# Kernel tuning notes

Hardware: AMD Instinct MI355X
Metric: run time of the kernel (lower is better)

Reference implementation:

```python
import jax, jax.numpy as jnp
import numpy as np

NUM_HEADS = 16
D_K = 64
D_V = 64
D_MODEL = 1024


def setup_inputs() -> dict:
    key = jax.random.key(0)
    ks = jax.random.split(key, 11)
    B, S = 2, 2048
    s = 0.02
    return {
        "Q": jax.random.normal(ks[0], (B, S, D_MODEL), jnp.float32),
        "K": jax.random.normal(ks[1], (B, S, D_MODEL), jnp.float32),
        "V": jax.random.normal(ks[2], (B, S, D_MODEL), jnp.float32),
        "WQ": jax.random.normal(ks[3], (D_MODEL, NUM_HEADS * D_K), jnp.float32) * s,
        "bQ": jnp.zeros((NUM_HEADS * D_K,), jnp.float32),
        "WK": jax.random.normal(ks[4], (D_MODEL, NUM_HEADS * D_K), jnp.float32) * s,
        "bK": jnp.zeros((NUM_HEADS * D_K,), jnp.float32),
        "WV": jax.random.normal(ks[5], (D_MODEL, NUM_HEADS * D_V), jnp.float32) * s,
        "bV": jnp.zeros((NUM_HEADS * D_V,), jnp.float32),
        "WO": jax.random.normal(ks[6], (NUM_HEADS * D_V, D_MODEL), jnp.float32) * s,
        "bO": jnp.zeros((D_MODEL,), jnp.float32),
    }


def reference(Q, K, V, WQ, bQ, WK, bK, WV, bV, WO, bO):
    B = Q.shape[0]
    # linear projections, then split heads: [B, H, S, d]
    q = (Q @ WQ + bQ).reshape(B, -1, NUM_HEADS, D_K).transpose(0, 2, 1, 3)
    k = (K @ WK + bK).reshape(B, -1, NUM_HEADS, D_K).transpose(0, 2, 1, 3)
    v = (V @ WV + bV).reshape(B, -1, NUM_HEADS, D_V).transpose(0, 2, 1, 3)
    # unfused attention: full [B, H, Sq, Sk] score matrix
    scores = jnp.einsum("bhqd,bhkd->bhqk", q, k) / jnp.sqrt(jnp.float32(D_K))
    attn = jax.nn.softmax(scores, axis=-1)  # dropout is identity in eval mode
    out = jnp.einsum("bhqk,bhkd->bhqd", attn, v)
    out = out.transpose(0, 2, 1, 3).reshape(B, -1, NUM_HEADS * D_V)
    return out @ WO + bO
```

## Files before the change

### kernel.cpp

```cpp
#include <hip/hip_runtime.h>
#include <hip/hip_bf16.h>
#include <stdint.h>

#define BATCH 2
#define SEQ   2048
#define NH    16
#define DH    64
#define DM    1024
#define MR    (BATCH * SEQ)

typedef __bf16 bf16_t;
typedef bf16_t bf16x4 __attribute__((ext_vector_type(4)));
typedef bf16_t bf16x8 __attribute__((ext_vector_type(8)));
typedef float  f32x4  __attribute__((ext_vector_type(4)));
typedef float  f32x16 __attribute__((ext_vector_type(16)));

typedef const __attribute__((address_space(1))) void* gas_t;
typedef       __attribute__((address_space(3))) void* las_t;

__device__ __forceinline__ void gload16(const void* g, void* l) {
  __builtin_amdgcn_global_load_lds((gas_t)g, (las_t)l, 16, 0, 0);
}

__device__ __forceinline__ float fast_exp2(float x) {
#if __has_builtin(__builtin_amdgcn_exp2f)
  return __builtin_amdgcn_exp2f(x);
#else
  float r; asm volatile("v_exp_f32 %0, %1\n\ts_nop 1" : "=v"(r) : "v"(x)); return r;
#endif
}

__global__ __launch_bounds__(256) void cvt3_kernel(const float* __restrict__ x0,
                                                   const float* __restrict__ x1,
                                                   const float* __restrict__ x2,
                                                   bf16_t* __restrict__ y0,
                                                   bf16_t* __restrict__ y1,
                                                   bf16_t* __restrict__ y2, int n) {
  const int z = blockIdx.y;
  const float* x = z == 0 ? x0 : (z == 1 ? x1 : x2);
  bf16_t*      y = z == 0 ? y0 : (z == 1 ? y1 : y2);
  int i = (blockIdx.x * 256 + threadIdx.x) * 8;
  if (i + 8 <= n) {
    float4 a = *(const float4*)(x + i);
    float4 b = *(const float4*)(x + i + 4);
    bf16x8 o;
    o[0] = (bf16_t)a.x; o[1] = (bf16_t)a.y; o[2] = (bf16_t)a.z; o[3] = (bf16_t)a.w;
    o[4] = (bf16_t)b.x; o[5] = (bf16_t)b.y; o[6] = (bf16_t)b.z; o[7] = (bf16_t)b.w;
    *(bf16x8*)(y + i) = o;
  }
}

__global__ __launch_bounds__(256) void wtrans4_kernel(const float* __restrict__ W0,
                                                      const float* __restrict__ W1,
                                                      const float* __restrict__ W2,
                                                      const float* __restrict__ W3,
                                                      bf16_t* __restrict__ T0,
                                                      bf16_t* __restrict__ T1,
                                                      bf16_t* __restrict__ T2,
                                                      bf16_t* __restrict__ T3) {
  const int z = blockIdx.z;
  const float* W = z == 0 ? W0 : (z == 1 ? W1 : (z == 2 ? W2 : W3));
  bf16_t*     Wt = z == 0 ? T0 : (z == 1 ? T1 : (z == 2 ? T2 : T3));
  __shared__ bf16_t t[64][65];
  const int c0 = blockIdx.x * 64, r0 = blockIdx.y * 64;
  const int tid = threadIdx.x;
  const int r = tid >> 2, cc = (tid & 3) * 16;
  const float* src = W + (size_t)(r0 + r) * DM + c0 + cc;
#pragma unroll
  for (int i = 0; i < 16; ++i) t[r][cc + i] = (bf16_t)src[i];
  __syncthreads();
  bf16_t* dst = Wt + (size_t)(c0 + r) * DM + r0 + cc;
#pragma unroll
  for (int i = 0; i < 16; ++i) dst[i] = t[cc + i][r];
}

__global__ __launch_bounds__(256) void gemm3_kernel(
    const bf16_t* __restrict__ A0, const bf16_t* __restrict__ A1,
    const bf16_t* __restrict__ A2,
    const bf16_t* __restrict__ B0, const bf16_t* __restrict__ B1,
    const bf16_t* __restrict__ B2,
    const float* __restrict__ bi0, const float* __restrict__ bi1,
    const float* __restrict__ bi2,
    float s0, float s1, float s2,
    bf16_t* __restrict__ C0, bf16_t* __restrict__ C1, bf16_t* __restrict__ C2) {
  const int z = blockIdx.z;
  const bf16_t* A    = z == 0 ? A0 : (z == 1 ? A1 : A2);
  const bf16_t* Bt   = z == 0 ? B0 : (z == 1 ? B1 : B2);
  const float*  bias = z == 0 ? bi0 : (z == 1 ? bi1 : bi2);
  const float   scale = z == 0 ? s0 : (z == 1 ? s1 : s2);
  bf16_t*       C    = z == 0 ? C0 : (z == 1 ? C1 : C2);
  const int K = DM, N = DM;

  __shared__ __attribute__((aligned(16))) bf16_t As[128 * 64];
  __shared__ __attribute__((aligned(16))) bf16_t Bs[128 * 64];
  const int m0 = blockIdx.x * 128, n0 = blockIdx.y * 128;
  const int tid = threadIdx.x;
  const int wave = tid >> 6, lane = tid & 63;
  const int lm = lane & 15, lg = lane >> 4;
  const int wr = wave >> 1, wc = wave & 1;
  f32x4 acc[4][4];
#pragma unroll
  for (int a = 0; a < 4; ++a)
#pragma unroll
    for (int bb = 0; bb < 4; ++bb) acc[a][bb] = (f32x4){0.f, 0.f, 0.f, 0.f};

  for (int k0 = 0; k0 < K; k0 += 64) {
    __syncthreads();
#pragma unroll
    for (int i = 0; i < 4; ++i) {
      const int c = tid + i * 256;
      const int row = c >> 3, j = c & 7, js = j ^ (row & 7);
      gload16(A  + (size_t)(m0 + row) * K + k0 + js * 8,
              As + (size_t)(wave * 64 + i * 256) * 8);
      gload16(Bt + (size_t)(n0 + row) * K + k0 + js * 8,
              Bs + (size_t)(wave * 64 + i * 256) * 8);
    }
    asm volatile("s_waitcnt vmcnt(0)" ::: "memory");
    __syncthreads();
#pragma unroll
    for (int kk = 0; kk < 2; ++kk) {
      bf16x8 af[4], bfr[4];
#pragma unroll
      for (int t = 0; t < 4; ++t) {
        const int ra = wr * 64 + t * 16 + lm;
        af[t] = *(const bf16x8*)((const char*)As + ra * 128 +
                                 ((kk * 64 + lg * 16) ^ ((ra & 7) << 4)));
        const int rb = wc * 64 + t * 16 + lm;
        bfr[t] = *(const bf16x8*)((const char*)Bs + rb * 128 +
                                  ((kk * 64 + lg * 16) ^ ((rb & 7) << 4)));
      }
      __builtin_amdgcn_s_setprio(1);
#pragma unroll
      for (int mf = 0; mf < 4; ++mf)
#pragma unroll
        for (int nf = 0; nf < 4; ++nf)
          acc[mf][nf] = __builtin_amdgcn_mfma_f32_16x16x32_bf16(af[mf], bfr[nf],
                                                                acc[mf][nf], 0, 0, 0);
      __builtin_amdgcn_s_setprio(0);
    }
  }
#pragma unroll
  for (int mf = 0; mf < 4; ++mf)
#pragma unroll
    for (int nf = 0; nf < 4; ++nf) {
      const int col = n0 + wc * 64 + nf * 16 + lm;
      const float bv = bias[col];
#pragma unroll
      for (int i = 0; i < 4; ++i) {
        const int row = m0 + wr * 64 + mf * 16 + lg * 4 + i;
        const float val = (acc[mf][nf][i] + bv) * scale;
        size_t off;
        if (z == 0) {
          off = (size_t)row * N + col;
        } else {
          const int bb = row >> 11, s = row & (SEQ - 1);
          const int hh = col >> 6, d = col & 63;
          const size_t base = (size_t)(bb * NH + hh) * (SEQ * DH);
          if (z == 1) {
            off = base + ((((size_t)(s >> 6) * 2 + ((s >> 5) & 1)) * 4 + (d >> 4)) * 64
                          + ((d >> 3) & 1) * 32 + (s & 31)) * 8 + (d & 7);
          } else {
            off = base + ((((size_t)(s >> 6) * 2 + (d >> 5)) * 4 + ((s >> 4) & 3)) * 64
                          + ((s >> 3) & 1) * 32 + (d & 31)) * 8 + (s & 7);
          }
        }
        C[off] = (bf16_t)val;
      }
    }
}

template <int OUT_BF16>
__global__ __launch_bounds__(256) void gemm_kernel(const bf16_t* __restrict__ A,
                                                   const bf16_t* __restrict__ Bt,
                                                   const float* __restrict__ bias,
                                                   float scale,
                                                   void* __restrict__ Cv,
                                                   int K, int N) {
  __shared__ __attribute__((aligned(16))) bf16_t As[64 * 64];
  __shared__ __attribute__((aligned(16))) bf16_t Bs[128 * 64];
  const int m0 = blockIdx.x * 64, n0 = blockIdx.y * 128;
  const int tid = threadIdx.x;
  const int wave = tid >> 6, lane = tid & 63;
  const int lm = lane & 15, lg = lane >> 4;
  const int wr = wave >> 1, wc = wave & 1;
  f32x4 acc[2][4];
#pragma unroll
  for (int a = 0; a < 2; ++a)
#pragma unroll
    for (int bb = 0; bb < 4; ++bb) acc[a][bb] = (f32x4){0.f, 0.f, 0.f, 0.f};

  for (int k0 = 0; k0 < K; k0 += 64) {
    __syncthreads();
#pragma unroll
    for (int i = 0; i < 2; ++i) {
      const int c = tid + i * 256;
      const int row = c >> 3, j = c & 7, js = j ^ (row & 7);
      gload16(A + (size_t)(m0 + row) * K + k0 + js * 8,
              As + (size_t)(wave * 64 + i * 256) * 8);
    }
#pragma unroll
    for (int i = 0; i < 4; ++i) {
      const int c = tid + i * 256;
      const int row = c >> 3, j = c & 7, js = j ^ (row & 7);
      gload16(Bt + (size_t)(n0 + row) * K + k0 + js * 8,
              Bs + (size_t)(wave * 64 + i * 256) * 8);
    }
    asm volatile("s_waitcnt vmcnt(0)" ::: "memory");
    __syncthreads();
#pragma unroll
    for (int kk = 0; kk < 2; ++kk) {
      bf16x8 af[2], bfr[4];
#pragma unroll
      for (int t = 0; t < 2; ++t) {
        const int ra = wr * 32 + t * 16 + lm;
        af[t] = *(const bf16x8*)((const char*)As + ra * 128 +
                                 ((kk * 64 + lg * 16) ^ ((ra & 7) << 4)));
      }
#pragma unroll
      for (int t = 0; t < 4; ++t) {
        const int rb = wc * 64 + t * 16 + lm;
        bfr[t] = *(const bf16x8*)((const char*)Bs + rb * 128 +
                                  ((kk * 64 + lg * 16) ^ ((rb & 7) << 4)));
      }
      __builtin_amdgcn_s_setprio(1);
#pragma unroll
      for (int mf = 0; mf < 2; ++mf)
#pragma unroll
        for (int nf = 0; nf < 4; ++nf)
          acc[mf][nf] = __builtin_amdgcn_mfma_f32_16x16x32_bf16(af[mf], bfr[nf],
                                                                acc[mf][nf], 0, 0, 0);
      __builtin_amdgcn_s_setprio(0);
    }
  }
#pragma unroll
  for (int mf = 0; mf < 2; ++mf)
#pragma unroll
    for (int nf = 0; nf < 4; ++nf) {
      const int col = n0 + wc * 64 + nf * 16 + lm;
      const float bv = bias[col];
#pragma unroll
      for (int i = 0; i < 4; ++i) {
        const int row = m0 + wr * 32 + mf * 16 + lg * 4 + i;
        const float val = (acc[mf][nf][i] + bv) * scale;
        if (OUT_BF16) ((bf16_t*)Cv)[(size_t)row * N + col] = (bf16_t)val;
        else          ((float*)Cv)[(size_t)row * N + col] = val;
      }
    }
}

__device__ __forceinline__ void attn_iter5(const bf16x8 (&kf)[8],
                                           const bf16x8 (&qf)[4],
                                           const bf16_t* __restrict__ vbt,
                                           f32x16 (&acc0)[2],
                                           float& mrun, float& lrun,
                                           char* __restrict__ PsW,
                                           int lq, int hi, int lane) {
  bf16x8 vf[8];
#pragma unroll
  for (int i = 0; i < 8; ++i) vf[i] = *(const bf16x8*)(vbt + i * 512);

  f32x16 sc[2];
#pragma unroll
  for (int r = 0; r < 16; ++r) { sc[0][r] = 0.f; sc[1][r] = 0.f; }
  __builtin_amdgcn_s_setprio(1);
#pragma unroll
  for (int ds = 0; ds < 4; ++ds) {
    sc[0] = __builtin_amdgcn_mfma_f32_32x32x16_bf16(kf[ds],     qf[ds], sc[0], 0, 0, 0);
    sc[1] = __builtin_amdgcn_mfma_f32_32x32x16_bf16(kf[4 + ds], qf[ds], sc[1], 0, 0, 0);
  }
  __builtin_amdgcn_s_setprio(0);

  float ml = sc[0][0];
#pragma unroll
  for (int r = 1; r < 16; ++r) ml = fmaxf(ml, sc[0][r]);
#pragma unroll
  for (int r = 0; r < 16; ++r) ml = fmaxf(ml, sc[1][r]);
  ml = fmaxf(ml, __shfl_xor(ml, 32));
  const bool defer = __all(ml - mrun <= 8.0f);
  const float mn = defer ? mrun : fmaxf(mrun, ml);
#pragma unroll
  for (int kt = 0; kt < 2; ++kt)
#pragma unroll
    for (int r = 0; r < 16; ++r) sc[kt][r] = fast_exp2(sc[kt][r] - mn);
  float s = 0.f;
#pragma unroll
  for (int r = 0; r < 16; ++r) s += sc[0][r] + sc[1][r];
  s += __shfl_xor(s, 32);
  if (defer) {
    lrun += s;
  } else {
    const float alpha = fast_exp2(mrun - mn);
    mrun = mn;
    lrun = lrun * alpha + s;
#pragma unroll
    for (int r = 0; r < 16; ++r) {
      const float ar = __shfl(alpha, (r & 3) + 8 * (r >> 2) + 4 * hi);
      acc0[0][r] *= ar;
      acc0[1][r] *= ar;
    }
  }

#pragma unroll
  for (int kt = 0; kt < 2; ++kt)
#pragma unroll
    for (int g = 0; g < 4; ++g) {
      bf16x4 pw;
      pw[0] = (bf16_t)sc[kt][4 * g + 0]; pw[1] = (bf16_t)sc[kt][4 * g + 1];
      pw[2] = (bf16_t)sc[kt][4 * g + 2]; pw[3] = (bf16_t)sc[kt][4 * g + 3];
      *(bf16x4*)(PsW + lq * 128 +
                 ((kt * 64 + g * 16 + hi * 8) ^ ((lq & 7) << 4))) = pw;
    }

#pragma unroll
  for (int ks = 0; ks < 4; ++ks) {
    bf16x8 pf = *(const bf16x8*)(PsW + lq * 128 +
                                 ((ks * 32 + hi * 16) ^ ((lq & 7) << 4)));
    __builtin_amdgcn_s_setprio(1);
    acc0[0] = __builtin_amdgcn_mfma_f32_32x32x16_bf16(pf, vf[ks],     acc0[0], 0, 0, 0);
    acc0[1] = __builtin_amdgcn_mfma_f32_32x32x16_bf16(pf, vf[4 + ks], acc0[1], 0, 0, 0);
    __builtin_amdgcn_s_setprio(0);
  }
}

__global__ __launch_bounds__(256, 2) void flash_kernel(const bf16_t* __restrict__ q,
                                                       const bf16_t* __restrict__ kF,
                                                       const bf16_t* __restrict__ vF,
                                                       bf16_t* __restrict__ o) {
  __shared__ __attribute__((aligned(16))) bf16_t Ps[4][32 * 64];
  const int wg = blockIdx.x;
  const int swz = (wg & 7) * 64 + (wg >> 3);
  const int qt = swz & 15, h = (swz >> 4) & 15, b = swz >> 8;
  const int tid = threadIdx.x;
  const int wave = tid >> 6, lane = tid & 63;
  const int lq = lane & 31, hi = lane >> 5;
  char* PsW = (char*)(&Ps[wave][0]);

  const bf16_t* qb = q + (size_t)(b * SEQ + qt * 128 + wave * 32) * DM + h * DH;
  const bf16_t* kb = kF + (size_t)(b * NH + h) * (SEQ * DH) + lane * 8;
  const bf16_t* vb = vF + (size_t)(b * NH + h) * (SEQ * DH) + lane * 8;

  bf16x8 qf[4];
#pragma unroll
  for (int ds = 0; ds < 4; ++ds)
    qf[ds] = *(const bf16x8*)(qb + (size_t)lq * DM + ds * 16 + hi * 8);

  f32x16 acc[2];
#pragma unroll
  for (int r = 0; r < 16; ++r) { acc[0][r] = 0.f; acc[1][r] = 0.f; }
  float mrun = -1e30f, lrun = 0.f;

  bf16x8 kfA[8], kfB[8];
#pragma unroll
  for (int i = 0; i < 8; ++i) kfA[i] = *(const bf16x8*)(kb + i * 512);

  const int NT = SEQ / 64;
  for (int t = 0; t < NT; t += 2) {
#pragma unroll
    for (int i = 0; i < 8; ++i)
      kfB[i] = *(const bf16x8*)(kb + (size_t)(t + 1) * 4096 + i * 512);
    attn_iter5(kfA, qf, vb + (size_t)t * 4096, acc, mrun, lrun, PsW, lq, hi, lane);
    {
      const int tn = (t + 2 < NT) ? t + 2 : NT - 1;
#pragma unroll
      for (int i = 0; i < 8; ++i)
        kfA[i] = *(const bf16x8*)(kb + (size_t)tn * 4096 + i * 512);
    }
    attn_iter5(kfB, qf, vb + (size_t)(t + 1) * 4096, acc, mrun, lrun, PsW, lq, hi, lane);
  }

  const float inv = __builtin_amdgcn_rcpf(lrun);
#pragma unroll
  for (int r = 0; r < 16; ++r) {
    const int qrow = (r & 3) + 8 * (r >> 2) + 4 * hi;
    const float iv = __shfl(inv, qrow);
    const int row = b * SEQ + qt * 128 + wave * 32 + qrow;
#pragma unroll
    for (int dt = 0; dt < 2; ++dt) {
      const int col = h * DH + dt * 32 + lq;
      o[(size_t)row * DM + col] = (bf16_t)(acc[dt][r] * iv);
    }
  }
}

extern "C" void kernel_launch(void* const* d_in, const int* in_sizes, int n_in,
                              void* d_out, int out_size, void* d_ws, size_t ws_size,
                              hipStream_t stream) {
  (void)in_sizes; (void)n_in; (void)out_size; (void)ws_size;
  const float* Q  = (const float*)d_in[0];
  const float* Kx = (const float*)d_in[1];
  const float* V  = (const float*)d_in[2];
  const float* WQ = (const float*)d_in[3];
  const float* bQ = (const float*)d_in[4];
  const float* WK = (const float*)d_in[5];
  const float* bK = (const float*)d_in[6];
  const float* WV = (const float*)d_in[7];
  const float* bV = (const float*)d_in[8];
  const float* WO = (const float*)d_in[9];
  const float* bO = (const float*)d_in[10];

  const size_t MS  = (size_t)MR * DM;
  const size_t WSZ = (size_t)DM * DM;
  bf16_t* ws  = (bf16_t*)d_ws;
  bf16_t* Qb  = ws;
  bf16_t* Kb  = Qb + MS;
  bf16_t* Vb  = Kb + MS;
  bf16_t* WQt = Vb + MS;
  bf16_t* WKt = WQt + WSZ;
  bf16_t* WVt = WKt + WSZ;
  bf16_t* WOt = WVt + WSZ;
  bf16_t* qp  = WOt + WSZ;
  bf16_t* kp  = qp + MS;
  bf16_t* vp  = kp + MS;
  bf16_t* ao  = Kb;

  const float scale_q = 0.125f * 1.44269504088896340736f;

  cvt3_kernel<<<dim3((unsigned)(MS / 2048), 3), 256, 0, stream>>>(Q, Kx, V, Qb, Kb, Vb, (int)MS);
  wtrans4_kernel<<<dim3(16, 16, 4), 256, 0, stream>>>(WQ, WK, WV, WO, WQt, WKt, WVt, WOt);

  gemm3_kernel<<<dim3(32, 8, 3), 256, 0, stream>>>(Qb, Kb, Vb,
                                                   WQt, WKt, WVt,
                                                   bQ, bK, bV,
                                                   scale_q, 1.0f, 1.0f,
                                                   qp, kp, vp);

  flash_kernel<<<dim3(512), 256, 0, stream>>>(qp, kp, vp, ao);
  gemm_kernel<0><<<dim3(MR / 64, DM / 128), 256, 0, stream>>>(ao, WOt, bO, 1.0f, d_out, DM, DM);
}
```

Measured before the change: 132.7 us.

## Fuse fp32-to-bf16 input conversion into QKV GEMM and pipeline flash K/V loads

```diff
diff --git a/kernel.cpp b/kernel.cpp
--- a/kernel.cpp
+++ b/kernel.cpp
@@ -30,25 +30,10 @@
 #endif
 }
 
-__global__ __launch_bounds__(256) void cvt3_kernel(const float* __restrict__ x0,
-                                                   const float* __restrict__ x1,
-                                                   const float* __restrict__ x2,
-                                                   bf16_t* __restrict__ y0,
-                                                   bf16_t* __restrict__ y1,
-                                                   bf16_t* __restrict__ y2, int n) {
-  const int z = blockIdx.y;
-  const float* x = z == 0 ? x0 : (z == 1 ? x1 : x2);
-  bf16_t*      y = z == 0 ? y0 : (z == 1 ? y1 : y2);
-  int i = (blockIdx.x * 256 + threadIdx.x) * 8;
-  if (i + 8 <= n) {
-    float4 a = *(const float4*)(x + i);
-    float4 b = *(const float4*)(x + i + 4);
-    bf16x8 o;
-    o[0] = (bf16_t)a.x; o[1] = (bf16_t)a.y; o[2] = (bf16_t)a.z; o[3] = (bf16_t)a.w;
-    o[4] = (bf16_t)b.x; o[5] = (bf16_t)b.y; o[6] = (bf16_t)b.z; o[7] = (bf16_t)b.w;
-    *(bf16x8*)(y + i) = o;
-  }
-}
+#define GL(dst, base, OFF) \
+  asm volatile("global_load_dwordx4 %0, %1, off offset:" #OFF : "=v"(dst) : "v"(base))
+#define WAITV(N) asm volatile("s_waitcnt vmcnt(" #N ")" ::: "memory")
+#define SCHED0 __builtin_amdgcn_sched_barrier(0)
 
 __global__ __launch_bounds__(256) void wtrans4_kernel(const float* __restrict__ W0,
                                                       const float* __restrict__ W1,
@@ -75,8 +60,8 @@
 }
 
 __global__ __launch_bounds__(256) void gemm3_kernel(
-    const bf16_t* __restrict__ A0, const bf16_t* __restrict__ A1,
-    const bf16_t* __restrict__ A2,
+    const float* __restrict__ A0, const float* __restrict__ A1,
+    const float* __restrict__ A2,
     const bf16_t* __restrict__ B0, const bf16_t* __restrict__ B1,
     const bf16_t* __restrict__ B2,
     const float* __restrict__ bi0, const float* __restrict__ bi1,
@@ -84,14 +69,14 @@
     float s0, float s1, float s2,
     bf16_t* __restrict__ C0, bf16_t* __restrict__ C1, bf16_t* __restrict__ C2) {
   const int z = blockIdx.z;
-  const bf16_t* A    = z == 0 ? A0 : (z == 1 ? A1 : A2);
+  const float*  A    = z == 0 ? A0 : (z == 1 ? A1 : A2);
   const bf16_t* Bt   = z == 0 ? B0 : (z == 1 ? B1 : B2);
   const float*  bias = z == 0 ? bi0 : (z == 1 ? bi1 : bi2);
   const float   scale = z == 0 ? s0 : (z == 1 ? s1 : s2);
   bf16_t*       C    = z == 0 ? C0 : (z == 1 ? C1 : C2);
   const int K = DM, N = DM;
 
-  __shared__ __attribute__((aligned(16))) bf16_t As[128 * 64];
+  __shared__ __attribute__((aligned(16))) float  As[128 * 64];
   __shared__ __attribute__((aligned(16))) bf16_t Bs[128 * 64];
   const int m0 = blockIdx.x * 128, n0 = blockIdx.y * 128;
   const int tid = threadIdx.x;
@@ -107,11 +92,16 @@
   for (int k0 = 0; k0 < K; k0 += 64) {
     __syncthreads();
 #pragma unroll
+    for (int i = 0; i < 8; ++i) {
+      const int c = tid + i * 256;
+      const int row = c >> 4, j = c & 15, js = j ^ (row & 15);
+      gload16(A + (size_t)(m0 + row) * K + k0 + js * 4,
+              As + (size_t)(wave * 64 + i * 256) * 4);
+    }
+#pragma unroll
     for (int i = 0; i < 4; ++i) {
       const int c = tid + i * 256;
       const int row = c >> 3, j = c & 7, js = j ^ (row & 7);
-      gload16(A  + (size_t)(m0 + row) * K + k0 + js * 8,
-              As + (size_t)(wave * 64 + i * 256) * 8);
       gload16(Bt + (size_t)(n0 + row) * K + k0 + js * 8,
               Bs + (size_t)(wave * 64 + i * 256) * 8);
     }
@@ -123,8 +113,15 @@
 #pragma unroll
       for (int t = 0; t < 4; ++t) {
         const int ra = wr * 64 + t * 16 + lm;
-        af[t] = *(const bf16x8*)((const char*)As + ra * 128 +
-                                 ((kk * 64 + lg * 16) ^ ((ra & 7) << 4)));
+        const char* arow = (const char*)As + ra * 256;
+        const int ca = kk * 8 + lg * 2;
+        f32x4 a0 = *(const f32x4*)(arow + (((ca    ) ^ (ra & 15)) << 4));
+        f32x4 a1 = *(const f32x4*)(arow + (((ca + 1) ^ (ra & 15)) << 4));
+#pragma unroll
+        for (int jj = 0; jj < 4; ++jj) {
+          af[t][jj]     = (bf16_t)a0[jj];
+          af[t][4 + jj] = (bf16_t)a1[jj];
+        }
         const int rb = wc * 64 + t * 16 + lm;
         bfr[t] = *(const bf16x8*)((const char*)Bs + rb * 128 +
                                   ((kk * 64 + lg * 16) ^ ((rb & 7) << 4)));
@@ -248,17 +245,18 @@
     }
 }
 
-__device__ __forceinline__ void attn_iter5(const bf16x8 (&kf)[8],
-                                           const bf16x8 (&qf)[4],
-                                           const bf16_t* __restrict__ vbt,
-                                           f32x16 (&acc0)[2],
-                                           float& mrun, float& lrun,
-                                           char* __restrict__ PsW,
-                                           int lq, int hi, int lane) {
-  bf16x8 vf[8];
-#pragma unroll
-  for (int i = 0; i < 8; ++i) vf[i] = *(const bf16x8*)(vbt + i * 512);
-
+__device__ __forceinline__ void issue8(bf16x8 (&f)[8], const bf16_t* p) {
+  const bf16_t* p2 = p + 2048;
+  GL(f[0], p, 0); GL(f[1], p, 1024); GL(f[2], p, 2048); GL(f[3], p, 3072);
+  GL(f[4], p2, 0); GL(f[5], p2, 1024); GL(f[6], p2, 2048); GL(f[7], p2, 3072);
+}
+
+__device__ __forceinline__ void qk_softmax_store(const bf16x8 (&kf)[8],
+                                                 const bf16x8 (&qf)[4],
+                                                 f32x16 (&acc)[2],
+                                                 float& mrun, float& lrun,
+                                                 char* __restrict__ PsW,
+                                                 int lq, int hi) {
   f32x16 sc[2];
 #pragma unroll
   for (int r = 0; r < 16; ++r) { sc[0][r] = 0.f; sc[1][r] = 0.f; }
@@ -295,8 +293,8 @@
 #pragma unroll
     for (int r = 0; r < 16; ++r) {
       const float ar = __shfl(alpha, (r & 3) + 8 * (r >> 2) + 4 * hi);
-      acc0[0][r] *= ar;
-      acc0[1][r] *= ar;
+      acc[0][r] *= ar;
+      acc[1][r] *= ar;
     }
   }
 
@@ -310,14 +308,17 @@
       *(bf16x4*)(PsW + lq * 128 +
                  ((kt * 64 + g * 16 + hi * 8) ^ ((lq & 7) << 4))) = pw;
     }
-
+}
+
+__device__ __forceinline__ void pv_step(const bf16x8 (&vf)[8], f32x16 (&acc)[2],
+                                        char* __restrict__ PsW, int lq, int hi) {
 #pragma unroll
   for (int ks = 0; ks < 4; ++ks) {
     bf16x8 pf = *(const bf16x8*)(PsW + lq * 128 +
                                  ((ks * 32 + hi * 16) ^ ((lq & 7) << 4)));
     __builtin_amdgcn_s_setprio(1);
-    acc0[0] = __builtin_amdgcn_mfma_f32_32x32x16_bf16(pf, vf[ks],     acc0[0], 0, 0, 0);
-    acc0[1] = __builtin_amdgcn_mfma_f32_32x32x16_bf16(pf, vf[4 + ks], acc0[1], 0, 0, 0);
+    acc[0] = __builtin_amdgcn_mfma_f32_32x32x16_bf16(pf, vf[ks],     acc[0], 0, 0, 0);
+    acc[1] = __builtin_amdgcn_mfma_f32_32x32x16_bf16(pf, vf[4 + ks], acc[1], 0, 0, 0);
     __builtin_amdgcn_s_setprio(0);
   }
 }
@@ -349,24 +350,28 @@
   for (int r = 0; r < 16; ++r) { acc[0][r] = 0.f; acc[1][r] = 0.f; }
   float mrun = -1e30f, lrun = 0.f;
 
-  bf16x8 kfA[8], kfB[8];
-#pragma unroll
-  for (int i = 0; i < 8; ++i) kfA[i] = *(const bf16x8*)(kb + i * 512);
+  bf16x8 kA[8], kB[8], vv[8];
+  issue8(kA, kb);
 
   const int NT = SEQ / 64;
   for (int t = 0; t < NT; t += 2) {
-#pragma unroll
-    for (int i = 0; i < 8; ++i)
-      kfB[i] = *(const bf16x8*)(kb + (size_t)(t + 1) * 4096 + i * 512);
-    attn_iter5(kfA, qf, vb + (size_t)t * 4096, acc, mrun, lrun, PsW, lq, hi, lane);
+    issue8(vv, vb + (size_t)t * 4096);
+    issue8(kB, kb + (size_t)(t + 1) * 4096);
+    WAITV(16); SCHED0;
+    qk_softmax_store(kA, qf, acc, mrun, lrun, PsW, lq, hi);
+    WAITV(8); SCHED0;
+    pv_step(vv, acc, PsW, lq, hi);
+    issue8(vv, vb + (size_t)(t + 1) * 4096);
     {
       const int tn = (t + 2 < NT) ? t + 2 : NT - 1;
-#pragma unroll
-      for (int i = 0; i < 8; ++i)
-        kfA[i] = *(const bf16x8*)(kb + (size_t)tn * 4096 + i * 512);
-    }
-    attn_iter5(kfB, qf, vb + (size_t)(t + 1) * 4096, acc, mrun, lrun, PsW, lq, hi, lane);
-  }
+      issue8(kA, kb + (size_t)tn * 4096);
+    }
+    WAITV(16); SCHED0;
+    qk_softmax_store(kB, qf, acc, mrun, lrun, PsW, lq, hi);
+    WAITV(8); SCHED0;
+    pv_step(vv, acc, PsW, lq, hi);
+  }
+  asm volatile("s_waitcnt vmcnt(0)" ::: "memory");
 
   const float inv = __builtin_amdgcn_rcpf(lrun);
 #pragma unroll
@@ -401,24 +406,20 @@
   const size_t MS  = (size_t)MR * DM;
   const size_t WSZ = (size_t)DM * DM;
   bf16_t* ws  = (bf16_t*)d_ws;
-  bf16_t* Qb  = ws;
-  bf16_t* Kb  = Qb + MS;
-  bf16_t* Vb  = Kb + MS;
-  bf16_t* WQt = Vb + MS;
+  bf16_t* WQt = ws;
   bf16_t* WKt = WQt + WSZ;
   bf16_t* WVt = WKt + WSZ;
   bf16_t* WOt = WVt + WSZ;
   bf16_t* qp  = WOt + WSZ;
   bf16_t* kp  = qp + MS;
   bf16_t* vp  = kp + MS;
-  bf16_t* ao  = Kb;
+  bf16_t* ao  = vp + MS;
 
   const float scale_q = 0.125f * 1.44269504088896340736f;
 
-  cvt3_kernel<<<dim3((unsigned)(MS / 2048), 3), 256, 0, stream>>>(Q, Kx, V, Qb, Kb, Vb, (int)MS);
   wtrans4_kernel<<<dim3(16, 16, 4), 256, 0, stream>>>(WQ, WK, WV, WO, WQt, WKt, WVt, WOt);
 
-  gemm3_kernel<<<dim3(32, 8, 3), 256, 0, stream>>>(Qb, Kb, Vb,
+  gemm3_kernel<<<dim3(32, 8, 3), 256, 0, stream>>>(Q, Kx, V,
                                                    WQt, WKt, WVt,
                                                    bQ, bK, bV,
                                                    scale_q, 1.0f, 1.0f,
```

Result: slower. 138.8 us (+4.6%).

## Split attention over key range with LDS-staged K/V and combine kernel

Applied to the files above, without the earlier changes.

```diff
diff --git a/kernel.cpp b/kernel.cpp
--- a/kernel.cpp
+++ b/kernel.cpp
@@ -8,6 +8,7 @@
 #define DH    64
 #define DM    1024
 #define MR    (BATCH * SEQ)
+#define BHS   65536
 
 typedef __bf16 bf16_t;
 typedef bf16_t bf16x4 __attribute__((ext_vector_type(4)));
@@ -29,6 +30,8 @@
   float r; asm volatile("v_exp_f32 %0, %1\n\ts_nop 1" : "=v"(r) : "v"(x)); return r;
 #endif
 }
+
+#define WAITV(N) asm volatile("s_waitcnt vmcnt(" #N ")" ::: "memory")
 
 __global__ __launch_bounds__(256) void cvt3_kernel(const float* __restrict__ x0,
                                                    const float* __restrict__ x1,
@@ -248,28 +251,10 @@
     }
 }
 
-__device__ __forceinline__ void attn_iter5(const bf16x8 (&kf)[8],
-                                           const bf16x8 (&qf)[4],
-                                           const bf16_t* __restrict__ vbt,
-                                           f32x16 (&acc0)[2],
-                                           float& mrun, float& lrun,
-                                           char* __restrict__ PsW,
-                                           int lq, int hi, int lane) {
-  bf16x8 vf[8];
-#pragma unroll
-  for (int i = 0; i < 8; ++i) vf[i] = *(const bf16x8*)(vbt + i * 512);
-
-  f32x16 sc[2];
-#pragma unroll
-  for (int r = 0; r < 16; ++r) { sc[0][r] = 0.f; sc[1][r] = 0.f; }
-  __builtin_amdgcn_s_setprio(1);
-#pragma unroll
-  for (int ds = 0; ds < 4; ++ds) {
-    sc[0] = __builtin_amdgcn_mfma_f32_32x32x16_bf16(kf[ds],     qf[ds], sc[0], 0, 0, 0);
-    sc[1] = __builtin_amdgcn_mfma_f32_32x32x16_bf16(kf[4 + ds], qf[ds], sc[1], 0, 0, 0);
-  }
-  __builtin_amdgcn_s_setprio(0);
-
+__device__ __forceinline__ void softmax_store(f32x16 (&sc)[2], f32x16 (&acc)[2],
+                                              float& mrun, float& lrun,
+                                              char* __restrict__ PsW,
+                                              int lq, int hi) {
   float ml = sc[0][0];
 #pragma unroll
   for (int r = 1; r < 16; ++r) ml = fmaxf(ml, sc[0][r]);
@@ -295,11 +280,10 @@
 #pragma unroll
     for (int r = 0; r < 16; ++r) {
       const float ar = __shfl(alpha, (r & 3) + 8 * (r >> 2) + 4 * hi);
-      acc0[0][r] *= ar;
-      acc0[1][r] *= ar;
-    }
-  }
-
+      acc[0][r] *= ar;
+      acc[1][r] *= ar;
+    }
+  }
 #pragma unroll
   for (int kt = 0; kt < 2; ++kt)
 #pragma unroll
@@ -310,34 +294,28 @@
       *(bf16x4*)(PsW + lq * 128 +
                  ((kt * 64 + g * 16 + hi * 8) ^ ((lq & 7) << 4))) = pw;
     }
-
-#pragma unroll
-  for (int ks = 0; ks < 4; ++ks) {
-    bf16x8 pf = *(const bf16x8*)(PsW + lq * 128 +
-                                 ((ks * 32 + hi * 16) ^ ((lq & 7) << 4)));
-    __builtin_amdgcn_s_setprio(1);
-    acc0[0] = __builtin_amdgcn_mfma_f32_32x32x16_bf16(pf, vf[ks],     acc0[0], 0, 0, 0);
-    acc0[1] = __builtin_amdgcn_mfma_f32_32x32x16_bf16(pf, vf[4 + ks], acc0[1], 0, 0, 0);
-    __builtin_amdgcn_s_setprio(0);
-  }
-}
-
-__global__ __launch_bounds__(256, 2) void flash_kernel(const bf16_t* __restrict__ q,
+}
+
+__global__ __launch_bounds__(256, 4) void flash_kernel(const bf16_t* __restrict__ q,
                                                        const bf16_t* __restrict__ kF,
                                                        const bf16_t* __restrict__ vF,
-                                                       bf16_t* __restrict__ o) {
-  __shared__ __attribute__((aligned(16))) bf16_t Ps[4][32 * 64];
+                                                       bf16_t* __restrict__ pacc,
+                                                       float* __restrict__ pml) {
+  __shared__ __attribute__((aligned(16))) bf16_t Ks[4096];
+  __shared__ __attribute__((aligned(16))) bf16_t Vs[4096];
+  __shared__ __attribute__((aligned(16))) bf16_t Ps[4][2048];
   const int wg = blockIdx.x;
-  const int swz = (wg & 7) * 64 + (wg >> 3);
-  const int qt = swz & 15, h = (swz >> 4) & 15, b = swz >> 8;
+  const int flat = (wg & 7) * 128 + (wg >> 3);
+  const int qt = flat & 15, h = (flat >> 4) & 15;
+  const int b = (flat >> 8) & 1, split = flat >> 9;
   const int tid = threadIdx.x;
   const int wave = tid >> 6, lane = tid & 63;
   const int lq = lane & 31, hi = lane >> 5;
   char* PsW = (char*)(&Ps[wave][0]);
 
   const bf16_t* qb = q + (size_t)(b * SEQ + qt * 128 + wave * 32) * DM + h * DH;
-  const bf16_t* kb = kF + (size_t)(b * NH + h) * (SEQ * DH) + lane * 8;
-  const bf16_t* vb = vF + (size_t)(b * NH + h) * (SEQ * DH) + lane * 8;
+  const bf16_t* ksrc = kF + (size_t)(b * NH + h) * (SEQ * DH) + tid * 8;
+  const bf16_t* vsrc = vF + (size_t)(b * NH + h) * (SEQ * DH) + tid * 8;
 
   bf16x8 qf[4];
 #pragma unroll
@@ -349,37 +327,83 @@
   for (int r = 0; r < 16; ++r) { acc[0][r] = 0.f; acc[1][r] = 0.f; }
   float mrun = -1e30f, lrun = 0.f;
 
-  bf16x8 kfA[8], kfB[8];
-#pragma unroll
-  for (int i = 0; i < 8; ++i) kfA[i] = *(const bf16x8*)(kb + i * 512);
-
-  const int NT = SEQ / 64;
-  for (int t = 0; t < NT; t += 2) {
-#pragma unroll
-    for (int i = 0; i < 8; ++i)
-      kfB[i] = *(const bf16x8*)(kb + (size_t)(t + 1) * 4096 + i * 512);
-    attn_iter5(kfA, qf, vb + (size_t)t * 4096, acc, mrun, lrun, PsW, lq, hi, lane);
-    {
-      const int tn = (t + 2 < NT) ? t + 2 : NT - 1;
-#pragma unroll
-      for (int i = 0; i < 8; ++i)
-        kfA[i] = *(const bf16x8*)(kb + (size_t)tn * 4096 + i * 512);
-    }
-    attn_iter5(kfB, qf, vb + (size_t)(t + 1) * 4096, acc, mrun, lrun, PsW, lq, hi, lane);
-  }
-
-  const float inv = __builtin_amdgcn_rcpf(lrun);
+  const int t0 = split * 16, tend = t0 + 16;
+
+  for (int t = t0; t < tend; ++t) {
+    gload16(ksrc + (size_t)t * 4096,        &Ks[wave * 512]);
+    gload16(ksrc + (size_t)t * 4096 + 2048, &Ks[2048 + wave * 512]);
+    gload16(vsrc + (size_t)t * 4096,        &Vs[wave * 512]);
+    gload16(vsrc + (size_t)t * 4096 + 2048, &Vs[2048 + wave * 512]);
+    WAITV(0);
+    __builtin_amdgcn_s_barrier();
+    asm volatile("" ::: "memory");
+
+    const char* Kb_ = (const char*)Ks;
+    const char* Vb_ = (const char*)Vs;
+
+    f32x16 sc[2];
+#pragma unroll
+    for (int r = 0; r < 16; ++r) { sc[0][r] = 0.f; sc[1][r] = 0.f; }
+    __builtin_amdgcn_s_setprio(1);
+#pragma unroll
+    for (int ds = 0; ds < 4; ++ds) {
+      bf16x8 k0 = *(const bf16x8*)(Kb_ + (0 * 4 + ds) * 1024 + lane * 16);
+      bf16x8 k1 = *(const bf16x8*)(Kb_ + (1 * 4 + ds) * 1024 + lane * 16);
+      sc[0] = __builtin_amdgcn_mfma_f32_32x32x16_bf16(k0, qf[ds], sc[0], 0, 0, 0);
+      sc[1] = __builtin_amdgcn_mfma_f32_32x32x16_bf16(k1, qf[ds], sc[1], 0, 0, 0);
+    }
+    __builtin_amdgcn_s_setprio(0);
+
+    softmax_store(sc, acc, mrun, lrun, PsW, lq, hi);
+
+#pragma unroll
+    for (int ks = 0; ks < 4; ++ks) {
+      bf16x8 pf = *(const bf16x8*)(PsW + lq * 128 +
+                                   ((ks * 32 + hi * 16) ^ ((lq & 7) << 4)));
+      bf16x8 v0 = *(const bf16x8*)(Vb_ + (0 * 4 + ks) * 1024 + lane * 16);
+      bf16x8 v1 = *(const bf16x8*)(Vb_ + (1 * 4 + ks) * 1024 + lane * 16);
+      __builtin_amdgcn_s_setprio(1);
+      acc[0] = __builtin_amdgcn_mfma_f32_32x32x16_bf16(pf, v0, acc[0], 0, 0, 0);
+      acc[1] = __builtin_amdgcn_mfma_f32_32x32x16_bf16(pf, v1, acc[1], 0, 0, 0);
+      __builtin_amdgcn_s_setprio(0);
+    }
+    asm volatile("" ::: "memory");
+    __builtin_amdgcn_s_barrier();
+  }
+
+  const size_t bhqbase = (size_t)(b * NH + h) * SEQ + qt * 128 + wave * 32;
+  bf16_t* pa = pacc + ((size_t)split * BHS + bhqbase) * 64;
 #pragma unroll
   for (int r = 0; r < 16; ++r) {
     const int qrow = (r & 3) + 8 * (r >> 2) + 4 * hi;
-    const float iv = __shfl(inv, qrow);
-    const int row = b * SEQ + qt * 128 + wave * 32 + qrow;
-#pragma unroll
-    for (int dt = 0; dt < 2; ++dt) {
-      const int col = h * DH + dt * 32 + lq;
-      o[(size_t)row * DM + col] = (bf16_t)(acc[dt][r] * iv);
-    }
-  }
+#pragma unroll
+    for (int dt = 0; dt < 2; ++dt)
+      pa[(size_t)qrow * 64 + dt * 32 + lq] = (bf16_t)acc[dt][r];
+  }
+  if (hi == 0) {
+    float2 v; v.x = mrun; v.y = lrun;
+    *(float2*)(pml + ((size_t)split * BHS + bhqbase + lq) * 2) = v;
+  }
+}
+
+__global__ __launch_bounds__(256) void combine_kernel(const bf16_t* __restrict__ pacc,
+                                                      const float* __restrict__ pml,
+                                                      bf16_t* __restrict__ ao) {
+  const int tid = blockIdx.x * 256 + threadIdx.x;
+  const int bhq = tid >> 3, d0 = (tid & 7) * 8;
+  const float2 ml0 = *(const float2*)(pml + (size_t)bhq * 2);
+  const float2 ml1 = *(const float2*)(pml + ((size_t)BHS + bhq) * 2);
+  const float M = fmaxf(ml0.x, ml1.x);
+  const float w0 = fast_exp2(ml0.x - M), w1 = fast_exp2(ml1.x - M);
+  const float inv = __builtin_amdgcn_rcpf(ml0.y * w0 + ml1.y * w1);
+  bf16x8 x0 = *(const bf16x8*)(pacc + (size_t)bhq * 64 + d0);
+  bf16x8 x1 = *(const bf16x8*)(pacc + (size_t)BHS * 64 + (size_t)bhq * 64 + d0);
+  const int qq = bhq & (SEQ - 1), hh = (bhq >> 11) & (NH - 1), bb = bhq >> 15;
+  bf16x8 o8;
+#pragma unroll
+  for (int j = 0; j < 8; ++j)
+    o8[j] = (bf16_t)(((float)x0[j] * w0 + (float)x1[j] * w1) * inv);
+  *(bf16x8*)(ao + (size_t)(bb * SEQ + qq) * DM + hh * DH + d0) = o8;
 }
 
 extern "C" void kernel_launch(void* const* d_in, const int* in_sizes, int n_in,
@@ -411,7 +435,9 @@
   bf16_t* qp  = WOt + WSZ;
   bf16_t* kp  = qp + MS;
   bf16_t* vp  = kp + MS;
-  bf16_t* ao  = Kb;
+  bf16_t* pacc = Qb;
+  bf16_t* ao  = Vb;
+  float*  pml = (float*)WQt;
 
   const float scale_q = 0.125f * 1.44269504088896340736f;
 
@@ -424,6 +450,7 @@
                                                    scale_q, 1.0f, 1.0f,
                                                    qp, kp, vp);
 
-  flash_kernel<<<dim3(512), 256, 0, stream>>>(qp, kp, vp, ao);
+  flash_kernel<<<dim3(1024), 256, 0, stream>>>(qp, kp, vp, pacc, pml);
+  combine_kernel<<<dim3(2048), 256, 0, stream>>>(pacc, pml, ao);
   gemm_kernel<0><<<dim3(MR / 64, DM / 128), 256, 0, stream>>>(ao, WOt, bO, 1.0f, d_out, DM, DM);
 }
```

Measured after the change: 136.2 us. 1.03x slower.
